# Performance work log

Hardware: AMD Instinct MI355X
Metric: run time of the kernel (lower is better)

The kernel has to match this reference:

```python
import jax, jax.numpy as jnp
import numpy as np

WS = 8            # window_size
SHIFT = WS // 2   # cyclic shift for 'SW' type
HEAD_DIM = 32
N_HEADS = 6       # input_dim // head_dim = 192 // 32
SCALE = HEAD_DIM ** -0.5


def _rel_index(ws):
    # relative position lookup indices, static
    cord = np.array([[i, j] for i in range(ws) for j in range(ws)])
    rel = cord[:, None, :] - cord[None, :, :] + ws - 1  # [p^2, p^2, 2]
    return rel[:, :, 0], rel[:, :, 1]


def _shift_mask(hw, ww, p, shift):
    # boolean mask for shifted windows, static (built in numpy)
    m = np.zeros((hw, ww, p, p, p, p), dtype=bool)
    s = p - shift
    m[-1, :, :s, :, s:, :] = True
    m[-1, :, s:, :, :s, :] = True
    m[:, -1, :, :s, :, s:] = True
    m[:, -1, :, s:, :, :s] = True
    # '(w1 w2) (p1 p2) (p3 p4)' with leading 1,1 broadcast dims
    return m.reshape(hw * ww, p * p, p * p)[None, None]


def setup_inputs() -> dict:
    key = jax.random.key(0)
    ks = jax.random.split(key, 6)
    B, H, W, C = 8, 256, 256, 192
    return {
        "x": jax.random.normal(ks[0], (B, H, W, C), dtype=jnp.float32),
        "w_qkv": jax.random.normal(ks[1], (C, 3 * C), dtype=jnp.float32) * 0.02,
        "b_qkv": jax.random.normal(ks[2], (3 * C,), dtype=jnp.float32) * 0.02,
        "rel_pos": jax.random.normal(ks[3], (N_HEADS, 2 * WS - 1, 2 * WS - 1), dtype=jnp.float32) * 0.02,
        "w_out": jax.random.normal(ks[4], (C, C), dtype=jnp.float32) * 0.02,
        "b_out": jax.random.normal(ks[5], (C,), dtype=jnp.float32) * 0.02,
    }


def reference(x, w_qkv, b_qkv, rel_pos, w_out, b_out):
    B, H, W, C = x.shape
    hw, ww = H // WS, W // WS
    nw, npx = hw * ww, WS * WS

    # cyclic shift (type != 'W')
    x = jnp.roll(x, (-SHIFT, -SHIFT), axis=(1, 2))
    # partition into windows: [B, nw, p^2, C]
    x = x.reshape(B, hw, WS, ww, WS, C).transpose(0, 1, 3, 2, 4, 5).reshape(B, nw, npx, C)

    qkv = x @ w_qkv + b_qkv                              # [B, nw, p^2, 3*h*d]
    qkv = qkv.reshape(B, nw, npx, 3 * N_HEADS, HEAD_DIM)
    qkv = jnp.moveaxis(qkv, 3, 0)                        # [3h, B, nw, p^2, d]
    q, k, v = qkv[:N_HEADS], qkv[N_HEADS:2 * N_HEADS], qkv[2 * N_HEADS:]

    sim = jnp.einsum('hbwpc,hbwqc->hbwpq', q, k) * SCALE  # [h, B, nw, p^2, p^2]
    ri, rj = _rel_index(WS)
    bias = rel_pos[:, ri, rj]                            # [h, p^2, p^2]
    sim = sim + bias[:, None, None]

    mask = jnp.asarray(_shift_mask(hw, ww, WS, SHIFT))   # [1, 1, nw, p^2, p^2]
    sim = jnp.where(mask, -jnp.inf, sim)

    probs = jax.nn.softmax(sim, axis=-1)
    out = jnp.einsum('hbwpq,hbwqc->hbwpc', probs, v)     # [h, B, nw, p^2, d]
    out = jnp.moveaxis(out, 0, 3).reshape(B, nw, npx, N_HEADS * HEAD_DIM)
    out = out @ w_out + b_out

    # un-window and reverse shift
    out = out.reshape(B, hw, ww, WS, WS, -1).transpose(0, 1, 3, 2, 4, 5).reshape(B, H, W, -1)
    return jnp.roll(out, (SHIFT, SHIFT), axis=(1, 2))
```

## Files before the change

kernel.cpp:

```cpp
#include <hip/hip_runtime.h>
#include <math.h>

#define WSZ 8
#define SHIFT 4
#define HD 32
#define NH 6
#define CH 192
#define HP 256
#define WP 256
#define NPX 64
#define SCALE 0.17677669529663687f

using bf16x8 = __attribute__((ext_vector_type(8))) short;
using f32x4  = __attribute__((ext_vector_type(4))) float;
using u16x4  = __attribute__((ext_vector_type(4))) unsigned short;
using u16x8  = __attribute__((ext_vector_type(8))) unsigned short;

#define MFMA __builtin_amdgcn_mfma_f32_16x16x32_bf16

__device__ __forceinline__ unsigned short f2bf(float f) {
    unsigned u = __float_as_uint(f);
    u += 0x7fffu + ((u >> 16) & 1u);
    return (unsigned short)(u >> 16);
}
__device__ __forceinline__ float bf2f(unsigned short h) {
    return __uint_as_float(((unsigned)h) << 16);
}

__global__ void wprep(const float* __restrict__ w_qkv,
                      const float* __restrict__ w_out,
                      unsigned short* __restrict__ ws)
{
    int idx = blockIdx.x * 256 + threadIdx.x;
    unsigned short* wqh = ws;
    unsigned short* wql = ws + 110592;
    unsigned short* woh = ws + 221184;
    unsigned short* wol = ws + 258048;
    if (idx < 110592) {
        int n = idx / 192, c = idx % 192;
        float v = w_qkv[c * 576 + n];
        unsigned short h = f2bf(v);
        wqh[idx] = h;
        wql[idx] = f2bf(v - bf2f(h));
    } else {
        int j = idx - 110592;
        int n = j / 192, c = j % 192;
        float v = w_out[c * 192 + n];
        unsigned short h = f2bf(v);
        woh[j] = h;
        wol[j] = f2bf(v - bf2f(h));
    }
}

__global__ __launch_bounds__(512)
void wmsa_mfma(const float* __restrict__ x,
               const float* __restrict__ b_qkv,
               const float* __restrict__ rel_pos,
               const float* __restrict__ b_out,
               const unsigned short* __restrict__ ws,
               float* __restrict__ out)
{
    __shared__ __align__(16) unsigned short xa_h[NPX][200];
    __shared__ __align__(16) unsigned short xa_l[NPX][200];
    __shared__ __align__(16) unsigned short qS[NPX][40], qL[NPX][40];
    __shared__ __align__(16) unsigned short kS[NPX][40], kL[NPX][40];
    __shared__ __align__(16) unsigned short vS[HD][72],  vL[HD][72];
    __shared__ __align__(16) float          simb[NPX][68];
    __shared__ __align__(16) unsigned short pS[NPX][72], pL[NPX][72];

    const unsigned short* wqh = ws;
    const unsigned short* wql = ws + 110592;
    const unsigned short* woh = ws + 221184;
    const unsigned short* wol = ws + 258048;

    const int t   = threadIdx.x;
    const int blk = blockIdx.x;
    const int b   = blk >> 10;
    const int w   = blk & 1023;
    const int wy  = w >> 5;
    const int wx  = w & 31;

    const int l   = t & 63;
    const int wv  = t >> 6;
    const int l15 = l & 15;
    const int lhi = l >> 4;
    const int g   = wv & 1;
    const int mt  = wv >> 1;

    #pragma unroll
    for (int i = 0; i < 6; ++i) {
        int idx = t + i * 512;
        int p   = idx / 48;
        int c4  = idx % 48;
        int py = p >> 3, px = p & 7;
        int sy = (wy * WSZ + py + SHIFT) & 255;
        int sx = (wx * WSZ + px + SHIFT) & 255;
        const float4* src = (const float4*)(x + (((size_t)b * HP + sy) * WP + sx) * CH);
        float4 v4 = src[c4];
        float f[4] = {v4.x, v4.y, v4.z, v4.w};
        u16x4 hi, lo;
        #pragma unroll
        for (int j = 0; j < 4; ++j) {
            unsigned short hh = f2bf(f[j]);
            hi[j] = hh;
            lo[j] = f2bf(f[j] - bf2f(hh));
        }
        *(u16x4*)&xa_h[p][c4 * 4] = hi;
        *(u16x4*)&xa_l[p][c4 * 4] = lo;
    }
    __syncthreads();

    const bool edgeY = (wy == 31);
    const bool edgeX = (wx == 31);
    const f32x4 zero4 = {0.f, 0.f, 0.f, 0.f};

    f32x4 att[NH];

    #pragma unroll
    for (int h = 0; h < NH; ++h) {
        {
            f32x4 acc[3] = {zero4, zero4, zero4};
            int wr[3]; int cl[3]; bool isv[3];
            #pragma unroll
            for (int tl = 0; tl < 3; ++tl) {
                int nl = g * 3 + tl;
                if (nl < 2)      { wr[tl] = h * 32 + nl * 16;             cl[tl] = nl * 16;       isv[tl] = false; }
                else if (nl < 4) { wr[tl] = 192 + h * 32 + (nl - 2) * 16; cl[tl] = (nl - 2) * 16; isv[tl] = false; }
                else             { wr[tl] = 384 + h * 32 + (nl - 4) * 16; cl[tl] = (nl - 4) * 16; isv[tl] = true;  }
            }
            #pragma unroll
            for (int kc = 0; kc < 6; ++kc) {
                bf16x8 axh = *(const bf16x8*)&xa_h[mt * 16 + l15][kc * 32 + lhi * 8];
                bf16x8 axl = *(const bf16x8*)&xa_l[mt * 16 + l15][kc * 32 + lhi * 8];
                #pragma unroll
                for (int tl = 0; tl < 3; ++tl) {
                    size_t wo = (size_t)(wr[tl] + l15) * 192 + kc * 32 + lhi * 8;
                    bf16x8 bwh = *(const bf16x8*)&wqh[wo];
                    bf16x8 bwl = *(const bf16x8*)&wql[wo];
                    if (!isv[tl]) {
                        acc[tl] = MFMA(bwh, axh, acc[tl], 0, 0, 0);
                        acc[tl] = MFMA(bwl, axh, acc[tl], 0, 0, 0);
                        acc[tl] = MFMA(bwh, axl, acc[tl], 0, 0, 0);
                    } else {
                        acc[tl] = MFMA(axh, bwh, acc[tl], 0, 0, 0);
                        acc[tl] = MFMA(axl, bwh, acc[tl], 0, 0, 0);
                        acc[tl] = MFMA(axh, bwl, acc[tl], 0, 0, 0);
                    }
                }
            }
            #pragma unroll
            for (int tl = 0; tl < 3; ++tl) {
                int nl = g * 3 + tl;
                if (!isv[tl]) {
                    int pix = mt * 16 + l15;
                    int c0  = cl[tl] + lhi * 4;
                    int jb  = (nl < 2 ? h * 32 : 192 + h * 32) + c0;
                    const f32x4 bias = *(const f32x4*)&b_qkv[jb];
                    u16x4 hi, lo;
                    #pragma unroll
                    for (int r = 0; r < 4; ++r) {
                        float v = acc[tl][r] + bias[r];
                        unsigned short hh = f2bf(v);
                        hi[r] = hh; lo[r] = f2bf(v - bf2f(hh));
                    }
                    if (nl < 2) { *(u16x4*)&qS[pix][c0] = hi; *(u16x4*)&qL[pix][c0] = lo; }
                    else        { *(u16x4*)&kS[pix][c0] = hi; *(u16x4*)&kL[pix][c0] = lo; }
                } else {
                    int d    = cl[tl] + l15;
                    int pix0 = mt * 16 + lhi * 4;
                    float bv = b_qkv[384 + h * 32 + d];
                    u16x4 hi, lo;
                    #pragma unroll
                    for (int r = 0; r < 4; ++r) {
                        float v = acc[tl][r] + bv;
                        unsigned short hh = f2bf(v);
                        hi[r] = hh; lo[r] = f2bf(v - bf2f(hh));
                    }
                    *(u16x4*)&vS[d][pix0] = hi;
                    *(u16x4*)&vL[d][pix0] = lo;
                }
            }
        }
        __syncthreads();

        {
            bf16x8 aqh = *(const bf16x8*)&qS[mt * 16 + l15][lhi * 8];
            bf16x8 aql = *(const bf16x8*)&qL[mt * 16 + l15][lhi * 8];
            #pragma unroll
            for (int k2 = 0; k2 < 2; ++k2) {
                int kt = g * 2 + k2;
                bf16x8 bkh = *(const bf16x8*)&kS[kt * 16 + l15][lhi * 8];
                bf16x8 bkl = *(const bf16x8*)&kL[kt * 16 + l15][lhi * 8];
                f32x4 s = zero4;
                s = MFMA(bkh, aqh, s, 0, 0, 0);
                s = MFMA(bkl, aqh, s, 0, 0, 0);
                s = MFMA(bkh, aql, s, 0, 0, 0);
                *(f32x4*)&simb[mt * 16 + l15][kt * 16 + lhi * 4] = s;
            }
        }
        __syncthreads();

        {
            const int p  = t >> 3;
            const int qb = (t & 7) * 8;
            const int py = p >> 3, px = p & 7;
            float s[8];
            f32x4 s0 = *(const f32x4*)&simb[p][qb];
            f32x4 s1 = *(const f32x4*)&simb[p][qb + 4];
            #pragma unroll
            for (int i = 0; i < 4; ++i) { s[i] = s0[i]; s[i + 4] = s1[i]; }
            #pragma unroll
            for (int i = 0; i < 8; ++i) {
                int q  = qb + i;
                int qy = q >> 3, qx = q & 7;
                float val = s[i] * SCALE + rel_pos[h * 225 + (py - qy + 7) * 15 + (px - qx + 7)];
                bool msk = (edgeY && ((py < SHIFT) != (qy < SHIFT))) ||
                           (edgeX && ((px < SHIFT) != (qx < SHIFT)));
                s[i] = msk ? -1e30f : val;
            }
            float m = s[0];
            #pragma unroll
            for (int i = 1; i < 8; ++i) m = fmaxf(m, s[i]);
            #pragma unroll
            for (int off = 1; off < 8; off <<= 1) m = fmaxf(m, __shfl_xor(m, off));
            float sum = 0.f;
            #pragma unroll
            for (int i = 0; i < 8; ++i) { s[i] = __expf(s[i] - m); sum += s[i]; }
            #pragma unroll
            for (int off = 1; off < 8; off <<= 1) sum += __shfl_xor(sum, off);
            float inv = 1.f / sum;
            u16x8 hi, lo;
            #pragma unroll
            for (int i = 0; i < 8; ++i) {
                float pv = s[i] * inv;
                unsigned short hh = f2bf(pv);
                hi[i] = hh; lo[i] = f2bf(pv - bf2f(hh));
            }
            *(u16x8*)&pS[p][qb] = hi;
            *(u16x8*)&pL[p][qb] = lo;
        }
        __syncthreads();

        {
            f32x4 pa = zero4;
            #pragma unroll
            for (int kc = 0; kc < 2; ++kc) {
                bf16x8 avh = *(const bf16x8*)&vS[g * 16 + l15][kc * 32 + lhi * 8];
                bf16x8 avl = *(const bf16x8*)&vL[g * 16 + l15][kc * 32 + lhi * 8];
                bf16x8 bph = *(const bf16x8*)&pS[mt * 16 + l15][kc * 32 + lhi * 8];
                bf16x8 bpl = *(const bf16x8*)&pL[mt * 16 + l15][kc * 32 + lhi * 8];
                pa = MFMA(avh, bph, pa, 0, 0, 0);
                pa = MFMA(avl, bph, pa, 0, 0, 0);
                pa = MFMA(avh, bpl, pa, 0, 0, 0);
            }
            att[h] = pa;
        }
        __syncthreads();
    }

    {
        int pix = mt * 16 + l15;
        #pragma unroll
        for (int h = 0; h < NH; ++h) {
            int c0 = h * 32 + g * 16 + lhi * 4;
            u16x4 hi, lo;
            #pragma unroll
            for (int r = 0; r < 4; ++r) {
                float v = att[h][r];
                unsigned short hh = f2bf(v);
                hi[r] = hh; lo[r] = f2bf(v - bf2f(hh));
            }
            *(u16x4*)&xa_h[pix][c0] = hi;
            *(u16x4*)&xa_l[pix][c0] = lo;
        }
    }
    __syncthreads();

    {
        f32x4 po[6];
        #pragma unroll
        for (int i = 0; i < 6; ++i) po[i] = zero4;
        #pragma unroll
        for (int kc = 0; kc < 6; ++kc) {
            bf16x8 bxh = *(const bf16x8*)&xa_h[mt * 16 + l15][kc * 32 + lhi * 8];
            bf16x8 bxl = *(const bf16x8*)&xa_l[mt * 16 + l15][kc * 32 + lhi * 8];
            #pragma unroll
            for (int tn = 0; tn < 6; ++tn) {
                int nt = g + 2 * tn;
                size_t wo = (size_t)(nt * 16 + l15) * 192 + kc * 32 + lhi * 8;
                bf16x8 awh = *(const bf16x8*)&woh[wo];
                bf16x8 awl = *(const bf16x8*)&wol[wo];
                po[tn] = MFMA(awh, bxh, po[tn], 0, 0, 0);
                po[tn] = MFMA(awl, bxh, po[tn], 0, 0, 0);
                po[tn] = MFMA(awh, bxl, po[tn], 0, 0, 0);
            }
        }
        int pix = mt * 16 + l15;
        int py = pix >> 3, px = pix & 7;
        int sy = (wy * WSZ + py + SHIFT) & 255;
        int sx = (wx * WSZ + px + SHIFT) & 255;
        float* dst = out + (((size_t)b * HP + sy) * WP + sx) * CH;
        #pragma unroll
        for (int tn = 0; tn < 6; ++tn) {
            int nt = g + 2 * tn;
            int c0 = nt * 16 + lhi * 4;
            f32x4 r = po[tn];
            const f32x4 bb = *(const f32x4*)&b_out[c0];
            r += bb;
            *(f32x4*)&dst[c0] = r;
        }
    }
}

extern "C" void kernel_launch(void* const* d_in, const int* in_sizes, int n_in,
                              void* d_out, int out_size, void* d_ws, size_t ws_size,
                              hipStream_t stream) {
    const float* x       = (const float*)d_in[0];
    const float* w_qkv   = (const float*)d_in[1];
    const float* b_qkv   = (const float*)d_in[2];
    const float* rel_pos = (const float*)d_in[3];
    const float* w_out   = (const float*)d_in[4];
    const float* b_out   = (const float*)d_in[5];
    unsigned short* ws   = (unsigned short*)d_ws;

    wprep<<<dim3(576), dim3(256), 0, stream>>>(w_qkv, w_out, ws);
    wmsa_mfma<<<dim3(8192), dim3(512), 0, stream>>>(
        x, b_qkv, rel_pos, b_out, ws, (float*)d_out);
}
```

Before: 3.145 ms.

## Keep input tile in registers and alias LDS buffers to raise occupancy

The input window tile is no longer staged in shared memory. Each lane loads and splits its own MFMA operand fragments from global memory straight into registers. The shared buffers are packed into one 64KB arena, with the output-projection staging aliased over the q/k/v region, and launch bounds request 4 waves per SIMD. The goal is to cut the LDS footprint and an initial barrier so more blocks fit per CU, at the cost of more live registers (12 bf16x8 vectors) and less coalesced global loads.

```diff
diff --git a/kernel.cpp b/kernel.cpp
--- a/kernel.cpp
+++ b/kernel.cpp
@@ -15,6 +15,7 @@
 using f32x4  = __attribute__((ext_vector_type(4))) float;
 using u16x4  = __attribute__((ext_vector_type(4))) unsigned short;
 using u16x8  = __attribute__((ext_vector_type(8))) unsigned short;
+typedef unsigned short ush;
 
 #define MFMA __builtin_amdgcn_mfma_f32_16x16x32_bf16
 
@@ -52,7 +53,7 @@
     }
 }
 
-__global__ __launch_bounds__(512)
+__global__ __launch_bounds__(512, 4)
 void wmsa_mfma(const float* __restrict__ x,
                const float* __restrict__ b_qkv,
                const float* __restrict__ rel_pos,
@@ -60,13 +61,18 @@
                const unsigned short* __restrict__ ws,
                float* __restrict__ out)
 {
-    __shared__ __align__(16) unsigned short xa_h[NPX][200];
-    __shared__ __align__(16) unsigned short xa_l[NPX][200];
-    __shared__ __align__(16) unsigned short qS[NPX][40], qL[NPX][40];
-    __shared__ __align__(16) unsigned short kS[NPX][40], kL[NPX][40];
-    __shared__ __align__(16) unsigned short vS[HD][72],  vL[HD][72];
-    __shared__ __align__(16) float          simb[NPX][68];
-    __shared__ __align__(16) unsigned short pS[NPX][72], pL[NPX][72];
+    __shared__ __align__(16) unsigned char lds_raw[65536];
+    ush   (*qS)[40]  = (ush  (*)[40])(lds_raw + 0);
+    ush   (*qL)[40]  = (ush  (*)[40])(lds_raw + 5120);
+    ush   (*kS)[40]  = (ush  (*)[40])(lds_raw + 10240);
+    ush   (*kL)[40]  = (ush  (*)[40])(lds_raw + 15360);
+    ush   (*vS)[72]  = (ush  (*)[72])(lds_raw + 20480);
+    ush   (*vL)[72]  = (ush  (*)[72])(lds_raw + 25088);
+    float (*simb)[68]= (float(*)[68])(lds_raw + 29696);
+    ush   (*pS)[72]  = (ush  (*)[72])(lds_raw + 47104);
+    ush   (*pL)[72]  = (ush  (*)[72])(lds_raw + 56320);
+    ush   (*aH)[200] = (ush  (*)[200])(lds_raw + 0);
+    ush   (*aL)[200] = (ush  (*)[200])(lds_raw + 25600);
 
     const unsigned short* wqh = ws;
     const unsigned short* wql = ws + 110592;
@@ -87,28 +93,29 @@
     const int g   = wv & 1;
     const int mt  = wv >> 1;
 
-    #pragma unroll
-    for (int i = 0; i < 6; ++i) {
-        int idx = t + i * 512;
-        int p   = idx / 48;
-        int c4  = idx % 48;
-        int py = p >> 3, px = p & 7;
-        int sy = (wy * WSZ + py + SHIFT) & 255;
-        int sx = (wx * WSZ + px + SHIFT) & 255;
-        const float4* src = (const float4*)(x + (((size_t)b * HP + sy) * WP + sx) * CH);
-        float4 v4 = src[c4];
-        float f[4] = {v4.x, v4.y, v4.z, v4.w};
-        u16x4 hi, lo;
-        #pragma unroll
-        for (int j = 0; j < 4; ++j) {
-            unsigned short hh = f2bf(f[j]);
-            hi[j] = hh;
-            lo[j] = f2bf(f[j] - bf2f(hh));
-        }
-        *(u16x4*)&xa_h[p][c4 * 4] = hi;
-        *(u16x4*)&xa_l[p][c4 * 4] = lo;
-    }
-    __syncthreads();
+    bf16x8 xh[6], xl[6];
+    {
+        const int pix = mt * 16 + l15;
+        const int py = pix >> 3, px = pix & 7;
+        const int sy = (wy * WSZ + py + SHIFT) & 255;
+        const int sx = (wx * WSZ + px + SHIFT) & 255;
+        const float* xp = x + (((size_t)b * HP + sy) * WP + sx) * CH;
+        #pragma unroll
+        for (int kc = 0; kc < 6; ++kc) {
+            float4 a0 = *(const float4*)(xp + kc * 32 + lhi * 8);
+            float4 a1 = *(const float4*)(xp + kc * 32 + lhi * 8 + 4);
+            float f[8] = {a0.x, a0.y, a0.z, a0.w, a1.x, a1.y, a1.z, a1.w};
+            bf16x8 hi, lo;
+            #pragma unroll
+            for (int j = 0; j < 8; ++j) {
+                unsigned short hh = f2bf(f[j]);
+                hi[j] = (short)hh;
+                lo[j] = (short)f2bf(f[j] - bf2f(hh));
+            }
+            xh[kc] = hi;
+            xl[kc] = lo;
+        }
+    }
 
     const bool edgeY = (wy == 31);
     const bool edgeX = (wx == 31);
@@ -130,8 +137,8 @@
             }
             #pragma unroll
             for (int kc = 0; kc < 6; ++kc) {
-                bf16x8 axh = *(const bf16x8*)&xa_h[mt * 16 + l15][kc * 32 + lhi * 8];
-                bf16x8 axl = *(const bf16x8*)&xa_l[mt * 16 + l15][kc * 32 + lhi * 8];
+                bf16x8 axh = xh[kc];
+                bf16x8 axl = xl[kc];
                 #pragma unroll
                 for (int tl = 0; tl < 3; ++tl) {
                     size_t wo = (size_t)(wr[tl] + l15) * 192 + kc * 32 + lhi * 8;
@@ -270,8 +277,8 @@
                 unsigned short hh = f2bf(v);
                 hi[r] = hh; lo[r] = f2bf(v - bf2f(hh));
             }
-            *(u16x4*)&xa_h[pix][c0] = hi;
-            *(u16x4*)&xa_l[pix][c0] = lo;
+            *(u16x4*)&aH[pix][c0] = hi;
+            *(u16x4*)&aL[pix][c0] = lo;
         }
     }
     __syncthreads();
@@ -282,8 +289,8 @@
         for (int i = 0; i < 6; ++i) po[i] = zero4;
         #pragma unroll
         for (int kc = 0; kc < 6; ++kc) {
-            bf16x8 bxh = *(const bf16x8*)&xa_h[mt * 16 + l15][kc * 32 + lhi * 8];
-            bf16x8 bxl = *(const bf16x8*)&xa_l[mt * 16 + l15][kc * 32 + lhi * 8];
+            bf16x8 bxh = *(const bf16x8*)&aH[mt * 16 + l15][kc * 32 + lhi * 8];
+            bf16x8 bxl = *(const bf16x8*)&aL[mt * 16 + l15][kc * 32 + lhi * 8];
             #pragma unroll
             for (int tn = 0; tn < 6; ++tn) {
                 int nt = g + 2 * tn;
```

New measurement: 2.907 ms. -7.6%, faster.
